# Performance work log

Hardware: AMD Instinct MI355X
Metric: run time of the kernel (lower is better)

## Reference

```python
import jax, jax.numpy as jnp
import numpy as np

EPS = 1e-12  # F.normalize default eps

def _l2norm(x, axis):
    n = jnp.sqrt(jnp.sum(x * x, axis=axis, keepdims=True))
    return x / jnp.maximum(n, EPS)

def setup_inputs() -> dict:
    key = jax.random.key(0)
    ks = jax.random.split(key, 6)
    N, C, K, B, OUT = 200000, 256, 64, 8, 1024
    alpha = 100.0
    feat = jax.random.normal(ks[0], (N, C), dtype=jnp.float32)
    batch_ids = jax.random.randint(ks[1], (N,), 0, B, dtype=jnp.int32)
    centroids = jax.random.uniform(ks[2], (K, C), dtype=jnp.float32)
    # _init_params: conv weight = 2*alpha*centroids, bias = -alpha*||centroid||_2
    conv_w = 2.0 * alpha * centroids
    conv_b = -alpha * jnp.sqrt(jnp.sum(centroids * centroids, axis=1))
    fc_w = jax.random.normal(ks[3], (OUT, K * C), dtype=jnp.float32) * (1.0 / np.sqrt(K * C))
    fc_b = jax.random.normal(ks[4], (OUT,), dtype=jnp.float32) * 0.01
    return {"feat": feat, "batch_ids": batch_ids, "centroids": centroids,
            "conv_w": conv_w, "conv_b": conv_b, "fc_w": fc_w, "fc_b": fc_b,
            "batch_size": B}

def reference(feat, batch_ids, centroids, conv_w, conv_b, fc_w, fc_b, batch_size):
    B = int(batch_size)
    K, C = centroids.shape
    # descriptor-wise L2 normalization (normalize_input=True)
    x = _l2norm(feat, axis=1)                       # [N, C]
    # 1x1 conv == linear: soft assignment logits per point
    logits = x @ conv_w.T + conv_b                  # [N, K]
    soft = jax.nn.softmax(logits, axis=1)           # [N, K]
    # Per-batch aggregation (replaces the python loop):
    # vlad[b,k,:] = sum_{p in b} soft[p,k] * x[p,:] - (sum_{p in b} soft[p,k]) * centroids[k,:]
    onehot = jax.nn.one_hot(batch_ids, B, dtype=x.dtype)          # [N, B]
    A = jnp.einsum('nb,nk,nc->bkc', onehot, soft, x)              # [B, K, C]
    S = jax.ops.segment_sum(soft, batch_ids, num_segments=B)      # [B, K]
    vlad = A - S[:, :, None] * centroids[None, :, :]              # [B, K, C]
    vlad = _l2norm(vlad, axis=2)                                  # intra-normalization over C
    v = vlad.reshape(B, K * C)
    out = v @ fc_w.T + fc_b                                       # [B, 1024]
    return _l2norm(out, axis=1)
```

## Files before the change

kernel.cpp:

```cpp
#include <hip/hip_runtime.h>
#include <hip/hip_bf16.h>

typedef __attribute__((ext_vector_type(8))) short bf16x8;
typedef __attribute__((ext_vector_type(4))) float f32x4;

#define PCAP 768

__device__ __forceinline__ void async_copy16(const void* g, void* l)
{
    __builtin_amdgcn_global_load_lds(
        (const __attribute__((address_space(1))) unsigned int*)g,
        (__attribute__((address_space(3))) unsigned int*)l, 16, 0, 0);
}

__global__ void p0_wsplit(const float* __restrict__ convw,
                          short* __restrict__ whi, short* __restrict__ wlo)
{
    int e = blockIdx.x * 256 + threadIdx.x;
    if (e >= 2048) return;
    int lane = e & 63;
    int kstep = (e >> 6) & 7;
    int nt = e >> 9;
    int cluster = nt * 16 + (lane & 15);
    int ch0 = kstep * 32 + (lane >> 4) * 8;
    const float* src = convw + cluster * 256 + ch0;
    #pragma unroll
    for (int j = 0; j < 8; ++j) {
        float x = src[j];
        unsigned u = __float_as_uint(x);
        unsigned uh = u & 0xffff0000u;
        float r = x - __uint_as_float(uh);
        whi[e * 8 + j] = (short)(u >> 16);
        wlo[e * 8 + j] = (short)(__float_as_uint(r) >> 16);
    }
}

__global__ __launch_bounds__(256, 3) void p1_mfma(
    const float* __restrict__ feat, const int* __restrict__ bids,
    const short* __restrict__ whi, const short* __restrict__ wlo,
    const float* __restrict__ convb,
    float* __restrict__ soft, float* __restrict__ invn, int* __restrict__ cnts, int N)
{
    __shared__ float xbuf[2][4096];
    __shared__ int cnt[8];
    const int t = threadIdx.x;
    if (t < 8) cnt[t] = 0;
    const int w = t >> 6, lane = t & 63;
    const int m = lane & 15, quad = lane >> 4;
    const int p0 = blockIdx.x * 64;

    int s_pt[4], s_inner[4];
    #pragma unroll
    for (int pass = 0; pass < 4; ++pass) {
        int slot = pass * 256 + t;
        s_pt[pass] = slot >> 4;
        s_inner[pass] = (slot & 15) ^ (s_pt[pass] & 15);
    }

    auto STAGE = [&](int bi, int ck) {
        #pragma unroll
        for (int pass = 0; pass < 4; ++pass) {
            int gpt = p0 + s_pt[pass];
            const float* src = (gpt < N)
                ? feat + (size_t)gpt * 256 + ck * 64 + s_inner[pass] * 4
                : feat;
            async_copy16(src, (char*)&xbuf[bi][0] + (size_t)(pass * 256 + w * 64) * 16);
        }
    };

    STAGE(0, 0);
    __syncthreads();

    f32x4 acc[4];
    #pragma unroll
    for (int nt = 0; nt < 4; ++nt) acc[nt] = (f32x4){0.f, 0.f, 0.f, 0.f};
    float ssq = 0.f;

    const bf16x8* WH = (const bf16x8*)whi;
    const bf16x8* WL = (const bf16x8*)wlo;
    const int ptl = w * 16 + m;

    #pragma unroll
    for (int ck = 0; ck < 4; ++ck) {
        bf16x8 wfh[2][4], wfl[2][4];
        #pragma unroll
        for (int k2 = 0; k2 < 2; ++k2)
            #pragma unroll
            for (int nt = 0; nt < 4; ++nt) {
                wfh[k2][nt] = WH[(nt * 8 + ck * 2 + k2) * 64 + lane];
                wfl[k2][nt] = WL[(nt * 8 + ck * 2 + k2) * 64 + lane];
            }
        __builtin_amdgcn_sched_barrier(0);
        if (ck < 3) STAGE((ck + 1) & 1, ck + 1);
        __builtin_amdgcn_sched_barrier(0);

        const float* B = &xbuf[ck & 1][0];
        #pragma unroll
        for (int k2 = 0; k2 < 2; ++k2) {
            int i0 = (k2 * 8 + quad * 2 + 0) ^ m;
            int i1 = (k2 * 8 + quad * 2 + 1) ^ m;
            float4 v0 = *(const float4*)(B + (ptl * 16 + i0) * 4);
            float4 v1 = *(const float4*)(B + (ptl * 16 + i1) * 4);
            float x[8] = {v0.x, v0.y, v0.z, v0.w, v1.x, v1.y, v1.z, v1.w};
            bf16x8 ahi, alo;
            #pragma unroll
            for (int j = 0; j < 8; ++j) {
                unsigned u = __float_as_uint(x[j]);
                float r = x[j] - __uint_as_float(u & 0xffff0000u);
                ahi[j] = (short)(u >> 16);
                alo[j] = (short)(__float_as_uint(r) >> 16);
                ssq += x[j] * x[j];
            }
            #pragma unroll
            for (int nt = 0; nt < 4; ++nt) {
                acc[nt] = __builtin_amdgcn_mfma_f32_16x16x32_bf16(ahi, wfh[k2][nt], acc[nt], 0, 0, 0);
                acc[nt] = __builtin_amdgcn_mfma_f32_16x16x32_bf16(ahi, wfl[k2][nt], acc[nt], 0, 0, 0);
                acc[nt] = __builtin_amdgcn_mfma_f32_16x16x32_bf16(alo, wfh[k2][nt], acc[nt], 0, 0, 0);
            }
        }
        if (ck < 3) __syncthreads();
    }

    ssq += __shfl_xor(ssq, 16);
    ssq += __shfl_xor(ssq, 32);

    float bias[4];
    #pragma unroll
    for (int nt = 0; nt < 4; ++nt) bias[nt] = convb[nt * 16 + m];

    #pragma unroll
    for (int r = 0; r < 4; ++r) {
        int pl = quad * 4 + r;
        int gpt = p0 + w * 16 + pl;
        float sq = __shfl(ssq, pl);
        float inv = rsqrtf(fmaxf(sq, 1e-24f));
        float v[4];
        #pragma unroll
        for (int nt = 0; nt < 4; ++nt) v[nt] = acc[nt][r] * inv + bias[nt];
        float mx = fmaxf(fmaxf(v[0], v[1]), fmaxf(v[2], v[3]));
        #pragma unroll
        for (int off = 8; off >= 1; off >>= 1) mx = fmaxf(mx, __shfl_xor(mx, off));
        float e[4];
        float s = 0.f;
        #pragma unroll
        for (int nt = 0; nt < 4; ++nt) { e[nt] = __expf(v[nt] - mx); s += e[nt]; }
        #pragma unroll
        for (int off = 8; off >= 1; off >>= 1) s += __shfl_xor(s, off);
        float rs = 1.0f / s;
        if (gpt < N) {
            #pragma unroll
            for (int nt = 0; nt < 4; ++nt)
                soft[(size_t)gpt * 64 + nt * 16 + m] = e[nt] * rs;
            if (m == 0) {
                invn[gpt] = inv;
                atomicAdd(&cnt[bids[gpt]], 1);
            }
        }
    }
    __syncthreads();
    if (t < 8) atomicAdd(&cnts[t], cnt[t]);
}

__global__ void p2_offsets(const int* __restrict__ cnts, int* __restrict__ offs, int* __restrict__ cur)
{
    if (threadIdx.x == 0) {
        int acc = 0;
        for (int b = 0; b < 8; ++b) { offs[b] = acc; cur[b] = acc; acc += cnts[b]; }
        offs[8] = acc;
    }
}

__global__ __launch_bounds__(256) void p2_scatter(
    const int* __restrict__ bids, int* __restrict__ cur, int* __restrict__ perm, int N)
{
    __shared__ int lcnt[8], lbase[8];
    const int t = threadIdx.x;
    if (t < 8) lcnt[t] = 0;
    __syncthreads();
    int p = blockIdx.x * 256 + t;
    int b = 0, my = 0;
    bool ok = p < N;
    if (ok) { b = bids[p]; my = atomicAdd(&lcnt[b], 1); }
    __syncthreads();
    if (t < 8) lbase[t] = atomicAdd(&cur[t], lcnt[t]);
    __syncthreads();
    if (ok) perm[lbase[b] + my] = p;
}

__global__ __launch_bounds__(256, 2) void p3_mfma(
    const float* __restrict__ feat, const float* __restrict__ soft,
    const float* __restrict__ invn, const int* __restrict__ perm,
    const int* __restrict__ offs, float* __restrict__ partial,
    float* __restrict__ S, int split)
{
    __shared__ short xsT_hi[256 * 32];
    __shared__ short xsT_lo[256 * 32];
    __shared__ short sT_hi[64 * 32];
    __shared__ short sT_lo[64 * 32];
    __shared__ int   pidxL[PCAP];
    __shared__ float invL[PCAP];

    const int b  = blockIdx.x / split;
    const int sp = blockIdx.x % split;
    const int start = offs[b], end = offs[b + 1];
    const int len = end - start;
    const int chunk = (len + split - 1) / split;
    const int s0 = start + sp * chunk;
    int myLen = end - s0;
    myLen = max(0, min(myLen, chunk));
    myLen = min(myLen, PCAP);

    const int t = threadIdx.x;
    const int w = t >> 6, lane = t & 63;
    const int m = lane & 15, quad = lane >> 4;

    for (int i = t; i < myLen; i += 256) pidxL[i] = perm[s0 + i];
    __syncthreads();
    for (int i = t; i < myLen; i += 256) invL[i] = invn[pidxL[i]];
    __syncthreads();

    f32x4 acc[16];
    #pragma unroll
    for (int ct = 0; ct < 16; ++ct) acc[ct] = (f32x4){0.f, 0.f, 0.f, 0.f};
    float sacc = 0.f;

    const int nch = (myLen + 31) >> 5;

    int   pids[8];
    float pinv[8];
    float xv[4][8];
    float sv[8];

    auto FETCH = [&](int q) {
        const int p0 = q * 32;
        #pragma unroll
        for (int j = 0; j < 8; ++j) {
            int pl = p0 + w * 8 + j;
            bool ok = pl < myLen;
            pids[j] = ok ? pidxL[pl] : -1;
            pinv[j] = ok ? invL[pl] : 0.f;
        }
        #pragma unroll
        for (int cg = 0; cg < 4; ++cg) {
            int c = cg * 64 + lane;
            #pragma unroll
            for (int j = 0; j < 8; ++j)
                xv[cg][j] = (pids[j] >= 0) ? feat[(size_t)pids[j] * 256 + c] : 0.f;
        }
        #pragma unroll
        for (int j = 0; j < 8; ++j)
            sv[j] = (pids[j] >= 0) ? soft[(size_t)pids[j] * 64 + lane] : 0.f;
    };

    if (nch > 0) FETCH(0);

    for (int q = 0; q < nch; ++q) {
        __syncthreads();
        #pragma unroll
        for (int cg = 0; cg < 4; ++cg) {
            int c = cg * 64 + lane;
            bf16x8 vh, vl;
            #pragma unroll
            for (int j = 0; j < 8; ++j) {
                float v = xv[cg][j] * pinv[j];
                unsigned u = __float_as_uint(v);
                float r = v - __uint_as_float(u & 0xffff0000u);
                vh[j] = (short)(u >> 16);
                vl[j] = (short)(__float_as_uint(r) >> 16);
            }
            int slot = (w ^ (c & 3)) * 8;
            *(bf16x8*)&xsT_hi[c * 32 + slot] = vh;
            *(bf16x8*)&xsT_lo[c * 32 + slot] = vl;
        }
        {
            bf16x8 vh, vl;
            #pragma unroll
            for (int j = 0; j < 8; ++j) {
                float v = sv[j];
                sacc += v;
                unsigned u = __float_as_uint(v);
                float r = v - __uint_as_float(u & 0xffff0000u);
                vh[j] = (short)(u >> 16);
                vl[j] = (short)(__float_as_uint(r) >> 16);
            }
            int slot = (w ^ (lane & 3)) * 8;
            *(bf16x8*)&sT_hi[lane * 32 + slot] = vh;
            *(bf16x8*)&sT_lo[lane * 32 + slot] = vl;
        }
        if (q + 1 < nch) FETCH(q + 1);
        __syncthreads();
        {
            const int arow = w * 16 + m;
            const int aslot = (quad ^ (m & 3)) * 8;
            bf16x8 ah = *(const bf16x8*)&sT_hi[arow * 32 + aslot];
            bf16x8 al = *(const bf16x8*)&sT_lo[arow * 32 + aslot];
            const int bslot = (quad ^ (m & 3)) * 8;
            #pragma unroll
            for (int ct = 0; ct < 16; ++ct) {
                const int brow = ct * 16 + m;
                bf16x8 bh = *(const bf16x8*)&xsT_hi[brow * 32 + bslot];
                bf16x8 bl = *(const bf16x8*)&xsT_lo[brow * 32 + bslot];
                acc[ct] = __builtin_amdgcn_mfma_f32_16x16x32_bf16(ah, bh, acc[ct], 0, 0, 0);
                acc[ct] = __builtin_amdgcn_mfma_f32_16x16x32_bf16(ah, bl, acc[ct], 0, 0, 0);
                acc[ct] = __builtin_amdgcn_mfma_f32_16x16x32_bf16(al, bh, acc[ct], 0, 0, 0);
            }
        }
    }

    float* dst = partial + (size_t)(b * split + sp) * 64 * 256;
    #pragma unroll
    for (int ct = 0; ct < 16; ++ct) {
        #pragma unroll
        for (int r = 0; r < 4; ++r) {
            int k = w * 16 + quad * 4 + r;
            dst[k * 256 + ct * 16 + m] = acc[ct][r];
        }
    }
    atomicAdd(S + b * 64 + lane, sacc);
}

__global__ __launch_bounds__(256) void p4a_vlad(
    const float* __restrict__ partial, const float* __restrict__ S,
    const float* __restrict__ cents, float* __restrict__ v, int split)
{
    const int b = blockIdx.x >> 6, k = blockIdx.x & 63;
    const int t = threadIdx.x;
    float sum = 0.f;
    const float* base = partial + ((size_t)(b * split) * 64 + k) * 256 + t;
    for (int sp = 0; sp < split; ++sp)
        sum += base[(size_t)sp * 64 * 256];
    float val = sum - S[b * 64 + k] * cents[k * 256 + t];
    float sq = val * val;
    #pragma unroll
    for (int off = 32; off >= 1; off >>= 1) sq += __shfl_xor(sq, off);
    __shared__ float wsum[4];
    if ((t & 63) == 0) wsum[t >> 6] = sq;
    __syncthreads();
    float tot = wsum[0] + wsum[1] + wsum[2] + wsum[3];
    float r = 1.0f / fmaxf(sqrtf(tot), 1e-12f);
    v[b * 16384 + k * 256 + t] = val * r;
}

__global__ __launch_bounds__(256) void p4b_fc(
    const float* __restrict__ v, const float* __restrict__ fcw,
    const float* __restrict__ fcb, float* __restrict__ pre)
{
    const int t = threadIdx.x;
    const int o0 = blockIdx.x * 4;
    float acc[4][8] = {};
    for (int it = 0; it < 64; ++it) {
        int i = it * 256 + t;
        float wv[4];
        #pragma unroll
        for (int oo = 0; oo < 4; ++oo) wv[oo] = fcw[(size_t)(o0 + oo) * 16384 + i];
        #pragma unroll
        for (int b = 0; b < 8; ++b) {
            float vv = v[b * 16384 + i];
            #pragma unroll
            for (int oo = 0; oo < 4; ++oo) acc[oo][b] += wv[oo] * vv;
        }
    }
    __shared__ float red[32][4];
    #pragma unroll
    for (int oo = 0; oo < 4; ++oo)
        #pragma unroll
        for (int b = 0; b < 8; ++b) {
            float sv = acc[oo][b];
            #pragma unroll
            for (int off = 32; off >= 1; off >>= 1) sv += __shfl_xor(sv, off);
            if ((t & 63) == 0) red[oo * 8 + b][t >> 6] = sv;
        }
    __syncthreads();
    if (t < 32) {
        int oo = t >> 3, b = t & 7;
        float sv = red[t][0] + red[t][1] + red[t][2] + red[t][3];
        pre[b * 1024 + o0 + oo] = sv + fcb[o0 + oo];
    }
}

__global__ __launch_bounds__(256) void p5_norm(const float* __restrict__ pre, float* __restrict__ out)
{
    const int b = blockIdx.x, t = threadIdx.x;
    float vals[4];
    float sq = 0.f;
    #pragma unroll
    for (int i = 0; i < 4; ++i) {
        vals[i] = pre[b * 1024 + t + 256 * i];
        sq += vals[i] * vals[i];
    }
    #pragma unroll
    for (int off = 32; off >= 1; off >>= 1) sq += __shfl_xor(sq, off);
    __shared__ float wsum[4];
    if ((t & 63) == 0) wsum[t >> 6] = sq;
    __syncthreads();
    float tot = wsum[0] + wsum[1] + wsum[2] + wsum[3];
    float r = 1.0f / fmaxf(sqrtf(tot), 1e-12f);
    #pragma unroll
    for (int i = 0; i < 4; ++i) out[b * 1024 + t + 256 * i] = vals[i] * r;
}

extern "C" void kernel_launch(void* const* d_in, const int* in_sizes, int n_in,
                              void* d_out, int out_size, void* d_ws, size_t ws_size,
                              hipStream_t stream)
{
    const float* feat  = (const float*)d_in[0];
    const int*   bids  = (const int*)d_in[1];
    const float* cents = (const float*)d_in[2];
    const float* convw = (const float*)d_in[3];
    const float* convb = (const float*)d_in[4];
    const float* fcw   = (const float*)d_in[5];
    const float* fcb   = (const float*)d_in[6];
    float* out = (float*)d_out;

    const int N = in_sizes[0] / 256;

    const size_t base_floats = 16384
                             + (size_t)N * 64  + N
                             + 512  + 8 * 16384  + 8192 ;
    const size_t base_ints = (size_t)N + 8 + 9 + 8;
    int split = 96;
    while (split > 16) {
        size_t tot = (base_floats + (size_t)split * 8 * 16384) * 4 + base_ints * 4;
        if (tot <= ws_size) break;
        split -= 16;
    }

    short* whi = (short*)d_ws;
    short* wlo = whi + 16384;
    float* soft = (float*)(wlo + 16384);
    float* invn = soft + (size_t)N * 64;
    float* partial = invn + N;
    float* S    = partial + (size_t)split * 8 * 16384;
    float* v    = S + 512;
    float* pre  = v + 8 * 16384;
    int* perm = (int*)(pre + 8192);
    int* cnts = perm + N;
    int* offs = cnts + 8;
    int* cur  = offs + 9;

    hipMemsetAsync(S, 0, 512 * sizeof(float), stream);
    hipMemsetAsync(cnts, 0, 8 * sizeof(int), stream);

    p0_wsplit<<<8, 256, 0, stream>>>(convw, whi, wlo);
    p1_mfma<<<(N + 63) / 64, 256, 0, stream>>>(feat, bids, whi, wlo, convb, soft, invn, cnts, N);
    p2_offsets<<<1, 64, 0, stream>>>(cnts, offs, cur);
    p2_scatter<<<(N + 255) / 256, 256, 0, stream>>>(bids, cur, perm, N);
    p3_mfma<<<8 * split, 256, 0, stream>>>(feat, soft, invn, perm, offs, partial, S, split);
    p4a_vlad<<<512, 256, 0, stream>>>(partial, S, cents, v, split);
    p4b_fc<<<256, 256, 0, stream>>>(v, fcw, fcb, pre);
    p5_norm<<<8, 256, 0, stream>>>(pre, out);
}
```

Measured before the change: 481.0 us.

## Stage split conv weights in LDS and load features directly into registers

The p1 kernel stops staging feature tiles through a double-buffered LDS pipeline. Each lane now loads its full 256-channel feature row from global memory into registers up front, and the pre-split hi/lo bf16 conv weights are copied asynchronously into LDS once per block. This removes the per-chunk barriers and the repeated per-wave global weight fetches, but it raises register pressure (16 float4 per lane) and LDS use (64KB), so launch bounds drop from 3 to 2 blocks per SM. The direct loads read 32-byte fragments per lane at a 1KB row stride, which may coalesce less well than the previous staging.

```diff
diff --git a/kernel.cpp b/kernel.cpp
--- a/kernel.cpp
+++ b/kernel.cpp
@@ -35,40 +35,39 @@
     }
 }
 
-__global__ __launch_bounds__(256, 3) void p1_mfma(
+__global__ __launch_bounds__(256, 2) void p1_mfma(
     const float* __restrict__ feat, const int* __restrict__ bids,
     const short* __restrict__ whi, const short* __restrict__ wlo,
     const float* __restrict__ convb,
     float* __restrict__ soft, float* __restrict__ invn, int* __restrict__ cnts, int N)
 {
-    __shared__ float xbuf[2][4096];
+    __shared__ short whL[2048 * 8];
+    __shared__ short wlL[2048 * 8];
     __shared__ int cnt[8];
     const int t = threadIdx.x;
     if (t < 8) cnt[t] = 0;
     const int w = t >> 6, lane = t & 63;
     const int m = lane & 15, quad = lane >> 4;
     const int p0 = blockIdx.x * 64;
-
-    int s_pt[4], s_inner[4];
-    #pragma unroll
-    for (int pass = 0; pass < 4; ++pass) {
-        int slot = pass * 256 + t;
-        s_pt[pass] = slot >> 4;
-        s_inner[pass] = (slot & 15) ^ (s_pt[pass] & 15);
-    }
-
-    auto STAGE = [&](int bi, int ck) {
-        #pragma unroll
-        for (int pass = 0; pass < 4; ++pass) {
-            int gpt = p0 + s_pt[pass];
-            const float* src = (gpt < N)
-                ? feat + (size_t)gpt * 256 + ck * 64 + s_inner[pass] * 4
-                : feat;
-            async_copy16(src, (char*)&xbuf[bi][0] + (size_t)(pass * 256 + w * 64) * 16);
-        }
-    };
-
-    STAGE(0, 0);
+    const int gp = p0 + w * 16 + m;
+    const bool valid = gp < N;
+
+    #pragma unroll
+    for (int pass = 0; pass < 8; ++pass) {
+        async_copy16((const bf16x8*)whi + pass * 256 + t,
+                     (char*)whL + (size_t)(pass * 256 + w * 64) * 16);
+        async_copy16((const bf16x8*)wlo + pass * 256 + t,
+                     (char*)wlL + (size_t)(pass * 256 + w * 64) * 16);
+    }
+
+    const float* frow = valid ? (feat + (size_t)gp * 256 + quad * 8) : feat;
+    float4 xv[16];
+    #pragma unroll
+    for (int ks = 0; ks < 8; ++ks) {
+        xv[2 * ks]     = *(const float4*)(frow + ks * 32);
+        xv[2 * ks + 1] = *(const float4*)(frow + ks * 32 + 4);
+    }
+
     __syncthreads();
 
     f32x4 acc[4];
@@ -76,49 +75,27 @@
     for (int nt = 0; nt < 4; ++nt) acc[nt] = (f32x4){0.f, 0.f, 0.f, 0.f};
     float ssq = 0.f;
 
-    const bf16x8* WH = (const bf16x8*)whi;
-    const bf16x8* WL = (const bf16x8*)wlo;
-    const int ptl = w * 16 + m;
-
-    #pragma unroll
-    for (int ck = 0; ck < 4; ++ck) {
-        bf16x8 wfh[2][4], wfl[2][4];
-        #pragma unroll
-        for (int k2 = 0; k2 < 2; ++k2)
-            #pragma unroll
-            for (int nt = 0; nt < 4; ++nt) {
-                wfh[k2][nt] = WH[(nt * 8 + ck * 2 + k2) * 64 + lane];
-                wfl[k2][nt] = WL[(nt * 8 + ck * 2 + k2) * 64 + lane];
-            }
-        __builtin_amdgcn_sched_barrier(0);
-        if (ck < 3) STAGE((ck + 1) & 1, ck + 1);
-        __builtin_amdgcn_sched_barrier(0);
-
-        const float* B = &xbuf[ck & 1][0];
-        #pragma unroll
-        for (int k2 = 0; k2 < 2; ++k2) {
-            int i0 = (k2 * 8 + quad * 2 + 0) ^ m;
-            int i1 = (k2 * 8 + quad * 2 + 1) ^ m;
-            float4 v0 = *(const float4*)(B + (ptl * 16 + i0) * 4);
-            float4 v1 = *(const float4*)(B + (ptl * 16 + i1) * 4);
-            float x[8] = {v0.x, v0.y, v0.z, v0.w, v1.x, v1.y, v1.z, v1.w};
-            bf16x8 ahi, alo;
-            #pragma unroll
-            for (int j = 0; j < 8; ++j) {
-                unsigned u = __float_as_uint(x[j]);
-                float r = x[j] - __uint_as_float(u & 0xffff0000u);
-                ahi[j] = (short)(u >> 16);
-                alo[j] = (short)(__float_as_uint(r) >> 16);
-                ssq += x[j] * x[j];
-            }
-            #pragma unroll
-            for (int nt = 0; nt < 4; ++nt) {
-                acc[nt] = __builtin_amdgcn_mfma_f32_16x16x32_bf16(ahi, wfh[k2][nt], acc[nt], 0, 0, 0);
-                acc[nt] = __builtin_amdgcn_mfma_f32_16x16x32_bf16(ahi, wfl[k2][nt], acc[nt], 0, 0, 0);
-                acc[nt] = __builtin_amdgcn_mfma_f32_16x16x32_bf16(alo, wfh[k2][nt], acc[nt], 0, 0, 0);
-            }
-        }
-        if (ck < 3) __syncthreads();
+    #pragma unroll
+    for (int ks = 0; ks < 8; ++ks) {
+        float x[8] = {xv[2 * ks].x, xv[2 * ks].y, xv[2 * ks].z, xv[2 * ks].w,
+                      xv[2 * ks + 1].x, xv[2 * ks + 1].y, xv[2 * ks + 1].z, xv[2 * ks + 1].w};
+        bf16x8 ahi, alo;
+        #pragma unroll
+        for (int j = 0; j < 8; ++j) {
+            unsigned u = __float_as_uint(x[j]);
+            float r = x[j] - __uint_as_float(u & 0xffff0000u);
+            ahi[j] = (short)(u >> 16);
+            alo[j] = (short)(__float_as_uint(r) >> 16);
+            ssq += x[j] * x[j];
+        }
+        #pragma unroll
+        for (int nt = 0; nt < 4; ++nt) {
+            bf16x8 bh = *(const bf16x8*)&whL[(size_t)((nt * 8 + ks) * 64 + lane) * 8];
+            bf16x8 bl = *(const bf16x8*)&wlL[(size_t)((nt * 8 + ks) * 64 + lane) * 8];
+            acc[nt] = __builtin_amdgcn_mfma_f32_16x16x32_bf16(ahi, bh, acc[nt], 0, 0, 0);
+            acc[nt] = __builtin_amdgcn_mfma_f32_16x16x32_bf16(ahi, bl, acc[nt], 0, 0, 0);
+            acc[nt] = __builtin_amdgcn_mfma_f32_16x16x32_bf16(alo, bh, acc[nt], 0, 0, 0);
+        }
     }
 
     ssq += __shfl_xor(ssq, 16);
```

Result: no change. 481.0 us (-0.0%).
